# Optimization experiments

Measured on AMD Instinct MI355X. Metric: run time of the kernel, lower is better.

Reference implementation:

```python
import jax, jax.numpy as jnp
import numpy as np

N_CODEBOOKS = 4
CODEBOOK_SIZE = 256
CODEBOOK_DIM = 64
COMMITMENT_COST = 0.25
SEM_PROJ = 64
W2V_DIM = 64
B, T = 64, 4096


def setup_inputs() -> dict:
    key = jax.random.key(0)
    ks = jax.random.split(key, 8)
    z = jax.random.normal(ks[0], (B, T, CODEBOOK_DIM), dtype=jnp.float32)
    w2v_targets = jax.random.normal(ks[1], (B, T, W2V_DIM), dtype=jnp.float32)
    # codebooks initialized uniform(-1/K, 1/K) as in torch init
    embeddings = jax.random.uniform(
        ks[2], (N_CODEBOOKS, CODEBOOK_SIZE, CODEBOOK_DIM), dtype=jnp.float32,
        minval=-1.0 / CODEBOOK_SIZE, maxval=1.0 / CODEBOOK_SIZE)
    s1 = 1.0 / np.sqrt(CODEBOOK_DIM)
    s2 = 1.0 / np.sqrt(SEM_PROJ)
    W1 = jax.random.uniform(ks[3], (CODEBOOK_DIM, SEM_PROJ), jnp.float32, -s1, s1)
    b1 = jax.random.uniform(ks[4], (SEM_PROJ,), jnp.float32, -s1, s1)
    W2 = jax.random.uniform(ks[5], (SEM_PROJ, W2V_DIM), jnp.float32, -s2, s2)
    b2 = jax.random.uniform(ks[6], (W2V_DIM,), jnp.float32, -s2, s2)
    return {"z": z, "w2v_targets": w2v_targets, "embeddings": embeddings,
            "W1": W1, "b1": b1, "W2": W2, "b2": b2}


def _vq(residual, E):
    # residual: [B,T,D], E: [K,D]
    Bb, Tt, D = residual.shape
    flat = residual.reshape(-1, D)  # [N,D]
    dist = (jnp.sum(flat * flat, axis=1, keepdims=True)
            - 2.0 * flat @ E.T
            + jnp.sum(E * E, axis=1))
    idx = jnp.argmin(dist, axis=1).reshape(Bb, Tt)  # [B,T]
    z_q = E[idx]  # gather -> [B,T,D]
    commit = jnp.mean((jax.lax.stop_gradient(z_q) - residual) ** 2)
    emb_l = jnp.mean((z_q - jax.lax.stop_gradient(residual)) ** 2)
    loss = emb_l + COMMITMENT_COST * commit
    z_q_st = residual + jax.lax.stop_gradient(z_q - residual)  # straight-through
    return z_q_st, idx, loss


def reference(z, w2v_targets, embeddings, W1, b1, W2, b2):
    residual = z
    z_q_total = jnp.zeros_like(z)
    codes = []
    vq_loss = jnp.float32(0.0)
    semantic_loss = jnp.float32(0.0)
    for i in range(embeddings.shape[0]):
        z_q_i, idx_i, loss_i = _vq(residual, embeddings[i])
        if i == 0:
            h = jax.nn.gelu(z_q_i @ W1 + b1, approximate=False)
            pred = h @ W2 + b2
            semantic_loss = jnp.mean((pred - w2v_targets) ** 2)
        z_q_total = z_q_total + z_q_i
        residual = residual - jax.lax.stop_gradient(z_q_i)
        codes.append(idx_i)
        vq_loss = vq_loss + loss_i
    all_codes = jnp.stack(codes, axis=-1)  # [B,T,n_codebooks]
    return z_q_total, all_codes, all_codes[..., 0], vq_loss, semantic_loss
```

## Files before the change

kernel.cpp:

```cpp
#include <hip/hip_runtime.h>
#include <math.h>

#define NCB 4
#define KC 256
#define DIM 64
#define NTOK (64*4096)
#define TPB 512
#define TOKB 128
#define HALF 128
#define MGRID (NTOK/TOKB)
#define GTPB 256
#define GBLK (NTOK/GTPB)

#define WS_C     0
#define WS_P     4096
#define WS_PVQ   69632
#define WS_PSEM  77824

#define ESTRIDE 68

#define ROWSQ(rr, A) { \
  float p0=rr[0]*rr[0], p1=rr[1]*rr[1], p2=rr[2]*rr[2], p3=rr[3]*rr[3]; \
  float p4=rr[4]*rr[4], p5=rr[5]*rr[5], p6=rr[6]*rr[6], p7=rr[7]*rr[7]; \
  _Pragma("unroll") \
  for (int m_ = 1; m_ < 8; ++m_) { \
    float s0=rr[8*m_+0]*rr[8*m_+0]; p0=p0+s0; float s1=rr[8*m_+1]*rr[8*m_+1]; p1=p1+s1; \
    float s2=rr[8*m_+2]*rr[8*m_+2]; p2=p2+s2; float s3=rr[8*m_+3]*rr[8*m_+3]; p3=p3+s3; \
    float s4=rr[8*m_+4]*rr[8*m_+4]; p4=p4+s4; float s5=rr[8*m_+5]*rr[8*m_+5]; p5=p5+s5; \
    float s6=rr[8*m_+6]*rr[8*m_+6]; p6=p6+s6; float s7=rr[8*m_+7]*rr[8*m_+7]; p7=p7+s7; \
  } \
  A = ((p0+p1) + (p2+p3)) + ((p4+p5) + (p6+p7)); }

__global__ __launch_bounds__(256) void precompute_kernel(
    const float* __restrict__ E,
    const float* __restrict__ W1, const float* __restrict__ b1,
    const float* __restrict__ W2, const float* __restrict__ b2,
    float* __restrict__ Cnp, float* __restrict__ P) {
#pragma clang fp contract(off)
    const int t = threadIdx.x;
    if (blockIdx.x == 0) {
        for (int i = 0; i < NCB; ++i) {
            const float* row = E + (size_t)(i*KC + t)*DIM;
            float e[DIM];
#pragma unroll
            for (int d = 0; d < DIM; ++d) e[d] = row[d];
            float A;
            ROWSQ(e, A);
            Cnp[i*KC + t] = A;
        }
    } else {
        const int c = t;
        float e[DIM];
#pragma unroll
        for (int d = 0; d < DIM; ++d) e[d] = E[(size_t)c*DIM + d];
        float h[DIM];
        for (int m = 0; m < DIM; ++m) {
            float acc = b1[m];
            for (int d = 0; d < DIM; ++d) acc = fmaf(e[d], W1[d*DIM + m], acc);
            h[m] = 0.5f * acc * (1.0f + erff(acc * 0.70710678118654752440f));
        }
        for (int n = 0; n < DIM; ++n) {
            float acc = b2[n];
            for (int m = 0; m < DIM; ++m) acc = fmaf(h[m], W2[m*DIM + n], acc);
            P[c*DIM + n] = acc;
        }
    }
}

__device__ __forceinline__ void scan_half(
    const int h, const int i, const int j,
    const float* __restrict__ e_lds, const float* __restrict__ r_lds,
    const float* __restrict__ C_lds, const float* __restrict__ A_lds,
    float* __restrict__ bv1_lds, int* __restrict__ bk1_lds,
    int* __restrict__ bk_lds) {
#pragma clang fp contract(off)
    float acc[4][8];
#pragma unroll
    for (int m = 0; m < 4; ++m)
#pragma unroll
        for (int n = 0; n < 8; ++n) acc[m][n] = 0.f;

#pragma unroll 1
    for (int c = 0; c < 16; ++c) {
        float4 e4[8];
#pragma unroll
        for (int n = 0; n < 8; ++n)
            e4[n] = *(const float4*)&e_lds[ESTRIDE*(j + 16*n) + 4*c];
#pragma unroll
        for (int m = 0; m < 4; ++m) {
            float4 r4 = *(const float4*)&r_lds[(c*TOKB + (i + 32*m))*4];
#pragma unroll
            for (int n = 0; n < 8; ++n) {
                acc[m][n] = fmaf(r4.x, e4[n].x, acc[m][n]);
                acc[m][n] = fmaf(r4.y, e4[n].y, acc[m][n]);
                acc[m][n] = fmaf(r4.z, e4[n].z, acc[m][n]);
                acc[m][n] = fmaf(r4.w, e4[n].w, acc[m][n]);
            }
        }
    }

    float Ck[8];
#pragma unroll
    for (int n = 0; n < 8; ++n) Ck[n] = C_lds[j + 16*n];

#pragma unroll
    for (int m = 0; m < 4; ++m) {
        const float A = A_lds[i + 32*m];
        float bv = INFINITY; int bk = 0;
#pragma unroll
        for (int n = 0; n < 8; ++n) {
            const int k = h*HALF + j + 16*n;
            const float x = fmaf(-2.0f, acc[m][n], A) + Ck[n];
            if (x < bv) { bv = x; bk = k; }
        }
#pragma unroll
        for (int s = 8; s >= 1; s >>= 1) {
            const float ov = __shfl_xor(bv, s);
            const int   ok = __shfl_xor(bk, s);
            if (ov < bv || (ov == bv && ok < bk)) { bv = ov; bk = ok; }
        }
        if (j == 0) {
            if (h == 0) { bv1_lds[i + 32*m] = bv; bk1_lds[i + 32*m] = bk; }
            else {
                const float v1 = bv1_lds[i + 32*m];
                const int   k1 = bk1_lds[i + 32*m];
                bk_lds[i + 32*m] = (bv < v1) ? bk : k1;
            }
        }
    }
}

__global__ __launch_bounds__(TPB, 4) void vq_main_kernel(
    const float* __restrict__ z, const float* __restrict__ Eg,
    const float* __restrict__ Cg,
    float* __restrict__ out_codes, float* __restrict__ out_codes0,
    float* __restrict__ partial_vq) {
#pragma clang fp contract(off)
    __shared__ float e_lds[HALF*ESTRIDE];
    __shared__ float r_lds[16*TOKB*4];
    __shared__ float A_lds[TOKB];
    __shared__ float C_lds[HALF];
    __shared__ int   bk_lds[TOKB];
    __shared__ float bv1_lds[TOKB];
    __shared__ int   bk1_lds[TOKB];
    __shared__ float red[TPB];

    const int t = threadIdx.x;
    const int j = t & 15;
    const int i = t >> 4;
    const int tokbase = blockIdx.x * TOKB;

    {
        const int tok = t >> 2;
        const int q0 = (t & 3) * 4;
        const float4* zp = (const float4*)(z + (size_t)(tokbase + tok)*DIM);
#pragma unroll
        for (int c = 0; c < 4; ++c) {
            float4 v = zp[q0 + c];
            *(float4*)&r_lds[((q0 + c)*TOKB + tok)*4] = v;
        }
    }
    __syncthreads();

    float vqacc = 0.f;
    int cs0 = 0, cs1 = 0, cs2 = 0, cs3 = 0;

#pragma unroll 1
    for (int cb = 0; cb < NCB; ++cb) {
        if (t < TOKB) {
            float rr[DIM];
#pragma unroll
            for (int c = 0; c < 16; ++c) {
                float4 v = *(const float4*)&r_lds[(c*TOKB + t)*4];
                rr[4*c+0]=v.x; rr[4*c+1]=v.y; rr[4*c+2]=v.z; rr[4*c+3]=v.w;
            }
            float A;
            ROWSQ(rr, A);
            A_lds[t] = A;
        }

        {
            const float* src = Eg + (size_t)cb*KC*DIM;
#pragma unroll
            for (int v = 0; v < 4; ++v) {
                const int idx = t*4 + v;
                const int row = idx >> 4, ch = idx & 15;
                *(float4*)&e_lds[ESTRIDE*row + 4*ch] =
                    *(const float4*)(src + row*DIM + 4*ch);
            }
            if (t < HALF) C_lds[t] = Cg[cb*KC + t];
        }
        __syncthreads();
        scan_half(0, i, j, e_lds, r_lds, C_lds, A_lds, bv1_lds, bk1_lds, bk_lds);
        __syncthreads();

        {
            const float* src = Eg + ((size_t)cb*KC + HALF)*DIM;
#pragma unroll
            for (int v = 0; v < 4; ++v) {
                const int idx = t*4 + v;
                const int row = idx >> 4, ch = idx & 15;
                *(float4*)&e_lds[ESTRIDE*row + 4*ch] =
                    *(const float4*)(src + row*DIM + 4*ch);
            }
            if (t < HALF) C_lds[t] = Cg[cb*KC + HALF + t];
        }
        __syncthreads();
        scan_half(1, i, j, e_lds, r_lds, C_lds, A_lds, bv1_lds, bk1_lds, bk_lds);
        __syncthreads();

        {
            const int tok = t >> 2;
            const int q0 = (t & 3) * 4;
            const int bk = bk_lds[tok];
            if ((t & 3) == 0) {
                if      (cb == 0) cs0 = bk;
                else if (cb == 1) cs1 = bk;
                else if (cb == 2) cs2 = bk;
                else              cs3 = bk;
            }
            const float* ep = Eg + ((size_t)cb*KC + bk)*DIM;
#pragma unroll
            for (int c = 0; c < 4; ++c) {
                float* rp = &r_lds[((q0 + c)*TOKB + tok)*4];
                float4 rv = *(const float4*)rp;
                float4 ev = *(const float4*)(ep + 4*(q0 + c));
                float tt, st;
                tt = ev.x - rv.x; vqacc = fmaf(tt,tt,vqacc); st = rv.x + tt; rv.x = rv.x - st;
                tt = ev.y - rv.y; vqacc = fmaf(tt,tt,vqacc); st = rv.y + tt; rv.y = rv.y - st;
                tt = ev.z - rv.z; vqacc = fmaf(tt,tt,vqacc); st = rv.z + tt; rv.z = rv.z - st;
                tt = ev.w - rv.w; vqacc = fmaf(tt,tt,vqacc); st = rv.w + tt; rv.w = rv.w - st;
                *(float4*)rp = rv;
            }
        }
        __syncthreads();
    }

    if ((t & 3) == 0) {
        const int tok = tokbase + (t >> 2);
        *(float4*)(out_codes + (size_t)tok*4) =
            make_float4((float)cs0, (float)cs1, (float)cs2, (float)cs3);
        out_codes0[tok] = (float)cs0;
    }

    red[t] = vqacc;
    __syncthreads();
    for (int off = TPB/2; off > 0; off >>= 1) {
        if (t < off) red[t] += red[t + off];
        __syncthreads();
    }
    if (t == 0) partial_vq[blockIdx.x] = red[0];
}

__global__ __launch_bounds__(GTPB) void gather_kernel(
    const float* __restrict__ codesf, const float* __restrict__ z,
    const float* __restrict__ Eg, const float* __restrict__ P,
    const float* __restrict__ w2v,
    float* __restrict__ zq, float* __restrict__ partial_sem) {
#pragma clang fp contract(off)
    __shared__ float red[GTPB];
    const int tid = threadIdx.x;
    const int tok = blockIdx.x * GTPB + tid;

    float4 cf = *(const float4*)(codesf + (size_t)tok*4);
    const int c0 = (int)cf.x, c1 = (int)cf.y, c2 = (int)cf.z, c3 = (int)cf.w;

    const float4* zp = (const float4*)(z + (size_t)tok*DIM);
    const float4* e0 = (const float4*)(Eg + (size_t)(0*KC + c0)*DIM);
    const float4* e1 = (const float4*)(Eg + (size_t)(1*KC + c1)*DIM);
    const float4* e2 = (const float4*)(Eg + (size_t)(2*KC + c2)*DIM);
    const float4* e3 = (const float4*)(Eg + (size_t)(3*KC + c3)*DIM);
    float4* o = (float4*)(zq + (size_t)tok*DIM);

    const float4* pp = (const float4*)(P + (size_t)c0*DIM);
    const float4* wv = (const float4*)(w2v + (size_t)tok*DIM);
    float sem = 0.f;

#pragma unroll
    for (int q = 0; q < 16; ++q) {
        float4 zv = zp[q], a = e0[q], b = e1[q], c = e2[q], d = e3[q];
        float4 out;
        {
            float rr, t, st, tot;
            rr = zv.x;
            t = a.x - rr; st = rr + t; tot = st;        rr = rr - st;
            t = b.x - rr; st = rr + t; tot = tot + st;  rr = rr - st;
            t = c.x - rr; st = rr + t; tot = tot + st;  rr = rr - st;
            t = d.x - rr; st = rr + t; tot = tot + st;
            out.x = tot;
        }
        {
            float rr, t, st, tot;
            rr = zv.y;
            t = a.y - rr; st = rr + t; tot = st;        rr = rr - st;
            t = b.y - rr; st = rr + t; tot = tot + st;  rr = rr - st;
            t = c.y - rr; st = rr + t; tot = tot + st;  rr = rr - st;
            t = d.y - rr; st = rr + t; tot = tot + st;
            out.y = tot;
        }
        {
            float rr, t, st, tot;
            rr = zv.z;
            t = a.z - rr; st = rr + t; tot = st;        rr = rr - st;
            t = b.z - rr; st = rr + t; tot = tot + st;  rr = rr - st;
            t = c.z - rr; st = rr + t; tot = tot + st;  rr = rr - st;
            t = d.z - rr; st = rr + t; tot = tot + st;
            out.z = tot;
        }
        {
            float rr, t, st, tot;
            rr = zv.w;
            t = a.w - rr; st = rr + t; tot = st;        rr = rr - st;
            t = b.w - rr; st = rr + t; tot = tot + st;  rr = rr - st;
            t = c.w - rr; st = rr + t; tot = tot + st;  rr = rr - st;
            t = d.w - rr; st = rr + t; tot = tot + st;
            out.w = tot;
        }
        o[q] = out;

        float4 pv = pp[q], wvv = wv[q];
        float df;
        df = pv.x - wvv.x; sem = fmaf(df, df, sem);
        df = pv.y - wvv.y; sem = fmaf(df, df, sem);
        df = pv.z - wvv.z; sem = fmaf(df, df, sem);
        df = pv.w - wvv.w; sem = fmaf(df, df, sem);
    }

    red[tid] = sem;
    __syncthreads();
    for (int off = GTPB/2; off > 0; off >>= 1) {
        if (tid < off) red[tid] += red[tid + off];
        __syncthreads();
    }
    if (tid == 0) partial_sem[blockIdx.x] = red[0];
}

__global__ __launch_bounds__(256) void reduce_kernel(
    const float* __restrict__ pvq, const float* __restrict__ psem,
    float* __restrict__ out_loss) {
    __shared__ float sv[256], ss[256];
    const int t = threadIdx.x;
    float a = 0.f, b = 0.f;
    for (int x = t; x < MGRID; x += 256) a += pvq[x];
    for (int x = t; x < GBLK; x += 256) b += psem[x];
    sv[t] = a; ss[t] = b;
    __syncthreads();
    for (int off = 128; off > 0; off >>= 1) {
        if (t < off) { sv[t] += sv[t+off]; ss[t] += ss[t+off]; }
        __syncthreads();
    }
    if (t == 0) {
        out_loss[0] = 1.25f * sv[0] / 16777216.0f;
        out_loss[1] = ss[0] / 16777216.0f;
    }
}

extern "C" void kernel_launch(void* const* d_in, const int* in_sizes, int n_in,
                              void* d_out, int out_size, void* d_ws, size_t ws_size,
                              hipStream_t stream) {
    (void)in_sizes; (void)n_in; (void)out_size; (void)ws_size;
    const float* z   = (const float*)d_in[0];
    const float* w2v = (const float*)d_in[1];
    const float* E   = (const float*)d_in[2];
    const float* W1  = (const float*)d_in[3];
    const float* b1  = (const float*)d_in[4];
    const float* W2  = (const float*)d_in[5];
    const float* b2  = (const float*)d_in[6];

    float* out = (float*)d_out;
    char*  ws  = (char*)d_ws;
    float* Cnp  = (float*)(ws + WS_C);
    float* P    = (float*)(ws + WS_P);
    float* pvq  = (float*)(ws + WS_PVQ);
    float* psem = (float*)(ws + WS_PSEM);

    float* out_zq     = out;
    float* out_codes  = out + 16777216;
    float* out_codes0 = out + 17825792;
    float* out_loss   = out + 18087936;

    precompute_kernel<<<2, 256, 0, stream>>>(E, W1, b1, W2, b2, Cnp, P);
    vq_main_kernel<<<MGRID, TPB, 0, stream>>>(z, E, Cnp, out_codes, out_codes0, pvq);
    gather_kernel<<<GBLK, GTPB, 0, stream>>>(out_codes, z, E, P, w2v, out_zq, psem);
    reduce_kernel<<<1, 256, 0, stream>>>(pvq, psem, out_loss);
}
```

Baseline: 723.1 us.

## Fuse gather/z_q reconstruction and semantic loss into the VQ main kernel

```diff
diff --git a/kernel.cpp b/kernel.cpp
--- a/kernel.cpp
+++ b/kernel.cpp
@@ -9,8 +9,6 @@
 #define TOKB 128
 #define HALF 128
 #define MGRID (NTOK/TOKB)
-#define GTPB 256
-#define GBLK (NTOK/GTPB)
 
 #define WS_C     0
 #define WS_P     4096
@@ -72,7 +70,7 @@
     const float* __restrict__ e_lds, const float* __restrict__ r_lds,
     const float* __restrict__ C_lds, const float* __restrict__ A_lds,
     float* __restrict__ bv1_lds, int* __restrict__ bk1_lds,
-    int* __restrict__ bk_lds) {
+    int* __restrict__ bk_out) {
 #pragma clang fp contract(off)
     float acc[4][8];
 #pragma unroll
@@ -82,19 +80,22 @@
 
 #pragma unroll 1
     for (int c = 0; c < 16; ++c) {
-        float4 e4[8];
-#pragma unroll
-        for (int n = 0; n < 8; ++n)
-            e4[n] = *(const float4*)&e_lds[ESTRIDE*(j + 16*n) + 4*c];
-#pragma unroll
-        for (int m = 0; m < 4; ++m) {
-            float4 r4 = *(const float4*)&r_lds[(c*TOKB + (i + 32*m))*4];
-#pragma unroll
-            for (int n = 0; n < 8; ++n) {
-                acc[m][n] = fmaf(r4.x, e4[n].x, acc[m][n]);
-                acc[m][n] = fmaf(r4.y, e4[n].y, acc[m][n]);
-                acc[m][n] = fmaf(r4.z, e4[n].z, acc[m][n]);
-                acc[m][n] = fmaf(r4.w, e4[n].w, acc[m][n]);
+#pragma unroll
+        for (int g = 0; g < 2; ++g) {
+            float4 e4[4];
+#pragma unroll
+            for (int n = 0; n < 4; ++n)
+                e4[n] = *(const float4*)&e_lds[ESTRIDE*(j + 16*(4*g + n)) + 4*c];
+#pragma unroll
+            for (int m = 0; m < 4; ++m) {
+                float4 r4 = *(const float4*)&r_lds[(c*TOKB + (i + 32*m))*4];
+#pragma unroll
+                for (int n = 0; n < 4; ++n) {
+                    acc[m][4*g+n] = fmaf(r4.x, e4[n].x, acc[m][4*g+n]);
+                    acc[m][4*g+n] = fmaf(r4.y, e4[n].y, acc[m][4*g+n]);
+                    acc[m][4*g+n] = fmaf(r4.z, e4[n].z, acc[m][4*g+n]);
+                    acc[m][4*g+n] = fmaf(r4.w, e4[n].w, acc[m][4*g+n]);
+                }
             }
         }
     }
@@ -124,7 +125,7 @@
             else {
                 const float v1 = bv1_lds[i + 32*m];
                 const int   k1 = bk1_lds[i + 32*m];
-                bk_lds[i + 32*m] = (bv < v1) ? bk : k1;
+                bk_out[i + 32*m] = (bv < v1) ? bk : k1;
             }
         }
     }
@@ -132,15 +133,17 @@
 
 __global__ __launch_bounds__(TPB, 4) void vq_main_kernel(
     const float* __restrict__ z, const float* __restrict__ Eg,
-    const float* __restrict__ Cg,
+    const float* __restrict__ Cg, const float* __restrict__ P,
+    const float* __restrict__ w2v,
     float* __restrict__ out_codes, float* __restrict__ out_codes0,
-    float* __restrict__ partial_vq) {
+    float* __restrict__ out_zq,
+    float* __restrict__ partial_vq, float* __restrict__ partial_sem) {
 #pragma clang fp contract(off)
     __shared__ float e_lds[HALF*ESTRIDE];
     __shared__ float r_lds[16*TOKB*4];
     __shared__ float A_lds[TOKB];
     __shared__ float C_lds[HALF];
-    __shared__ int   bk_lds[TOKB];
+    __shared__ int   bkall_lds[NCB][TOKB];
     __shared__ float bv1_lds[TOKB];
     __shared__ int   bk1_lds[TOKB];
     __shared__ float red[TPB];
@@ -163,7 +166,6 @@
     __syncthreads();
 
     float vqacc = 0.f;
-    int cs0 = 0, cs1 = 0, cs2 = 0, cs3 = 0;
 
 #pragma unroll 1
     for (int cb = 0; cb < NCB; ++cb) {
@@ -191,7 +193,8 @@
             if (t < HALF) C_lds[t] = Cg[cb*KC + t];
         }
         __syncthreads();
-        scan_half(0, i, j, e_lds, r_lds, C_lds, A_lds, bv1_lds, bk1_lds, bk_lds);
+        scan_half(0, i, j, e_lds, r_lds, C_lds, A_lds, bv1_lds, bk1_lds,
+                  &bkall_lds[cb][0]);
         __syncthreads();
 
         {
@@ -206,19 +209,14 @@
             if (t < HALF) C_lds[t] = Cg[cb*KC + HALF + t];
         }
         __syncthreads();
-        scan_half(1, i, j, e_lds, r_lds, C_lds, A_lds, bv1_lds, bk1_lds, bk_lds);
+        scan_half(1, i, j, e_lds, r_lds, C_lds, A_lds, bv1_lds, bk1_lds,
+                  &bkall_lds[cb][0]);
         __syncthreads();
 
         {
             const int tok = t >> 2;
             const int q0 = (t & 3) * 4;
-            const int bk = bk_lds[tok];
-            if ((t & 3) == 0) {
-                if      (cb == 0) cs0 = bk;
-                else if (cb == 1) cs1 = bk;
-                else if (cb == 2) cs2 = bk;
-                else              cs3 = bk;
-            }
+            const int bk = bkall_lds[cb][tok];
             const float* ep = Eg + ((size_t)cb*KC + bk)*DIM;
 #pragma unroll
             for (int c = 0; c < 4; ++c) {
@@ -236,11 +234,78 @@
         __syncthreads();
     }
 
-    if ((t & 3) == 0) {
-        const int tok = tokbase + (t >> 2);
-        *(float4*)(out_codes + (size_t)tok*4) =
-            make_float4((float)cs0, (float)cs1, (float)cs2, (float)cs3);
-        out_codes0[tok] = (float)cs0;
+    float sem = 0.f;
+    {
+        const int tok = t >> 2;
+        const int q0 = (t & 3) * 4;
+        const int gtok = tokbase + tok;
+        const int c0 = bkall_lds[0][tok], c1 = bkall_lds[1][tok];
+        const int c2 = bkall_lds[2][tok], c3 = bkall_lds[3][tok];
+
+        if ((t & 3) == 0) {
+            *(float4*)(out_codes + (size_t)gtok*4) =
+                make_float4((float)c0, (float)c1, (float)c2, (float)c3);
+            out_codes0[gtok] = (float)c0;
+        }
+
+        const float4* zp = (const float4*)(z + (size_t)gtok*DIM);
+        const float4* e0 = (const float4*)(Eg + (size_t)(0*KC + c0)*DIM);
+        const float4* e1 = (const float4*)(Eg + (size_t)(1*KC + c1)*DIM);
+        const float4* e2 = (const float4*)(Eg + (size_t)(2*KC + c2)*DIM);
+        const float4* e3 = (const float4*)(Eg + (size_t)(3*KC + c3)*DIM);
+        float4* o = (float4*)(out_zq + (size_t)gtok*DIM);
+        const float4* pp = (const float4*)(P + (size_t)c0*DIM);
+        const float4* wv = (const float4*)(w2v + (size_t)gtok*DIM);
+
+#pragma unroll
+        for (int q = q0; q < q0 + 4; ++q) {
+            float4 zv = zp[q], a = e0[q], b = e1[q], c = e2[q], d = e3[q];
+            float4 out;
+            {
+                float rr, tt, st, tot;
+                rr = zv.x;
+                tt = a.x - rr; st = rr + tt; tot = st;        rr = rr - st;
+                tt = b.x - rr; st = rr + tt; tot = tot + st;  rr = rr - st;
+                tt = c.x - rr; st = rr + tt; tot = tot + st;  rr = rr - st;
+                tt = d.x - rr; st = rr + tt; tot = tot + st;
+                out.x = tot;
+            }
+            {
+                float rr, tt, st, tot;
+                rr = zv.y;
+                tt = a.y - rr; st = rr + tt; tot = st;        rr = rr - st;
+                tt = b.y - rr; st = rr + tt; tot = tot + st;  rr = rr - st;
+                tt = c.y - rr; st = rr + tt; tot = tot + st;  rr = rr - st;
+                tt = d.y - rr; st = rr + tt; tot = tot + st;
+                out.y = tot;
+            }
+            {
+                float rr, tt, st, tot;
+                rr = zv.z;
+                tt = a.z - rr; st = rr + tt; tot = st;        rr = rr - st;
+                tt = b.z - rr; st = rr + tt; tot = tot + st;  rr = rr - st;
+                tt = c.z - rr; st = rr + tt; tot = tot + st;  rr = rr - st;
+                tt = d.z - rr; st = rr + tt; tot = tot + st;
+                out.z = tot;
+            }
+            {
+                float rr, tt, st, tot;
+                rr = zv.w;
+                tt = a.w - rr; st = rr + tt; tot = st;        rr = rr - st;
+                tt = b.w - rr; st = rr + tt; tot = tot + st;  rr = rr - st;
+                tt = c.w - rr; st = rr + tt; tot = tot + st;  rr = rr - st;
+                tt = d.w - rr; st = rr + tt; tot = tot + st;
+                out.w = tot;
+            }
+            o[q] = out;
+
+            float4 pv = pp[q], wvv = wv[q];
+            float df;
+            df = pv.x - wvv.x; sem = fmaf(df, df, sem);
+            df = pv.y - wvv.y; sem = fmaf(df, df, sem);
+            df = pv.z - wvv.z; sem = fmaf(df, df, sem);
+            df = pv.w - wvv.w; sem = fmaf(df, df, sem);
+        }
     }
 
     red[t] = vqacc;
@@ -250,89 +315,14 @@
         __syncthreads();
     }
     if (t == 0) partial_vq[blockIdx.x] = red[0];
-}
-
-__global__ __launch_bounds__(GTPB) void gather_kernel(
-    const float* __restrict__ codesf, const float* __restrict__ z,
-    const float* __restrict__ Eg, const float* __restrict__ P,
-    const float* __restrict__ w2v,
-    float* __restrict__ zq, float* __restrict__ partial_sem) {
-#pragma clang fp contract(off)
-    __shared__ float red[GTPB];
-    const int tid = threadIdx.x;
-    const int tok = blockIdx.x * GTPB + tid;
-
-    float4 cf = *(const float4*)(codesf + (size_t)tok*4);
-    const int c0 = (int)cf.x, c1 = (int)cf.y, c2 = (int)cf.z, c3 = (int)cf.w;
-
-    const float4* zp = (const float4*)(z + (size_t)tok*DIM);
-    const float4* e0 = (const float4*)(Eg + (size_t)(0*KC + c0)*DIM);
-    const float4* e1 = (const float4*)(Eg + (size_t)(1*KC + c1)*DIM);
-    const float4* e2 = (const float4*)(Eg + (size_t)(2*KC + c2)*DIM);
-    const float4* e3 = (const float4*)(Eg + (size_t)(3*KC + c3)*DIM);
-    float4* o = (float4*)(zq + (size_t)tok*DIM);
-
-    const float4* pp = (const float4*)(P + (size_t)c0*DIM);
-    const float4* wv = (const float4*)(w2v + (size_t)tok*DIM);
-    float sem = 0.f;
-
-#pragma unroll
-    for (int q = 0; q < 16; ++q) {
-        float4 zv = zp[q], a = e0[q], b = e1[q], c = e2[q], d = e3[q];
-        float4 out;
-        {
-            float rr, t, st, tot;
-            rr = zv.x;
-            t = a.x - rr; st = rr + t; tot = st;        rr = rr - st;
-            t = b.x - rr; st = rr + t; tot = tot + st;  rr = rr - st;
-            t = c.x - rr; st = rr + t; tot = tot + st;  rr = rr - st;
-            t = d.x - rr; st = rr + t; tot = tot + st;
-            out.x = tot;
-        }
-        {
-            float rr, t, st, tot;
-            rr = zv.y;
-            t = a.y - rr; st = rr + t; tot = st;        rr = rr - st;
-            t = b.y - rr; st = rr + t; tot = tot + st;  rr = rr - st;
-            t = c.y - rr; st = rr + t; tot = tot + st;  rr = rr - st;
-            t = d.y - rr; st = rr + t; tot = tot + st;
-            out.y = tot;
-        }
-        {
-            float rr, t, st, tot;
-            rr = zv.z;
-            t = a.z - rr; st = rr + t; tot = st;        rr = rr - st;
-            t = b.z - rr; st = rr + t; tot = tot + st;  rr = rr - st;
-            t = c.z - rr; st = rr + t; tot = tot + st;  rr = rr - st;
-            t = d.z - rr; st = rr + t; tot = tot + st;
-            out.z = tot;
-        }
-        {
-            float rr, t, st, tot;
-            rr = zv.w;
-            t = a.w - rr; st = rr + t; tot = st;        rr = rr - st;
-            t = b.w - rr; st = rr + t; tot = tot + st;  rr = rr - st;
-            t = c.w - rr; st = rr + t; tot = tot + st;  rr = rr - st;
-            t = d.w - rr; st = rr + t; tot = tot + st;
-            out.w = tot;
-        }
-        o[q] = out;
-
-        float4 pv = pp[q], wvv = wv[q];
-        float df;
-        df = pv.x - wvv.x; sem = fmaf(df, df, sem);
-        df = pv.y - wvv.y; sem = fmaf(df, df, sem);
-        df = pv.z - wvv.z; sem = fmaf(df, df, sem);
-        df = pv.w - wvv.w; sem = fmaf(df, df, sem);
-    }
-
-    red[tid] = sem;
-    __syncthreads();
-    for (int off = GTPB/2; off > 0; off >>= 1) {
-        if (tid < off) red[tid] += red[tid + off];
-        __syncthreads();
-    }
-    if (tid == 0) partial_sem[blockIdx.x] = red[0];
+    __syncthreads();
+    red[t] = sem;
+    __syncthreads();
+    for (int off = TPB/2; off > 0; off >>= 1) {
+        if (t < off) red[t] += red[t + off];
+        __syncthreads();
+    }
+    if (t == 0) partial_sem[blockIdx.x] = red[0];
 }
 
 __global__ __launch_bounds__(256) void reduce_kernel(
@@ -341,8 +331,7 @@
     __shared__ float sv[256], ss[256];
     const int t = threadIdx.x;
     float a = 0.f, b = 0.f;
-    for (int x = t; x < MGRID; x += 256) a += pvq[x];
-    for (int x = t; x < GBLK; x += 256) b += psem[x];
+    for (int x = t; x < MGRID; x += 256) { a += pvq[x]; b += psem[x]; }
     sv[t] = a; ss[t] = b;
     __syncthreads();
     for (int off = 128; off > 0; off >>= 1) {
@@ -380,7 +369,8 @@
     float* out_loss   = out + 18087936;
 
     precompute_kernel<<<2, 256, 0, stream>>>(E, W1, b1, W2, b2, Cnp, P);
-    vq_main_kernel<<<MGRID, TPB, 0, stream>>>(z, E, Cnp, out_codes, out_codes0, pvq);
-    gather_kernel<<<GBLK, GTPB, 0, stream>>>(out_codes, z, E, P, w2v, out_zq, psem);
+    vq_main_kernel<<<MGRID, TPB, 0, stream>>>(z, E, Cnp, P, w2v,
+                                              out_codes, out_codes0, out_zq,
+                                              pvq, psem);
     reduce_kernel<<<1, 256, 0, stream>>>(pvq, psem, out_loss);
 }
```

After: 586.9 us, median of 2. -18.8%, faster.
